# Kernel optimization log

Measured on AMD Instinct MI355X. Metric: run time of the kernel, lower is better.

Reference implementation:

```python
import jax, jax.numpy as jnp
import numpy as np

N = 50000   # nodes
E = 800000  # edges
IN, H, C = 256, 128, 4


def _gcn_norm(edge_index, n):
    """Add self-loops and compute symmetric GCN normalization per edge."""
    loops = jnp.arange(n, dtype=edge_index.dtype)
    src = jnp.concatenate([edge_index[0], loops])
    dst = jnp.concatenate([edge_index[1], loops])
    deg = jax.ops.segment_sum(jnp.ones_like(dst, dtype=jnp.float32), dst,
                              num_segments=n)
    dinv = jnp.where(deg > 0, jax.lax.rsqrt(deg), 0.0)
    norm = dinv[src] * dinv[dst]  # [E+N]
    return src, dst, norm


def _gcn_conv(h, src, dst, norm, W, b, n):
    h = h @ W                              # [N, out]
    msg = h[src] * norm[:, None]           # gather + scale, [E+N, out]
    agg = jax.ops.segment_sum(msg, dst, num_segments=n)
    return agg + b


def setup_inputs() -> dict:
    key = jax.random.key(0)
    ks = jax.random.split(key, 5)
    x = jax.random.normal(ks[0], (N, IN), dtype=jnp.float32)
    edge_index = jax.random.randint(ks[1], (2, E), 0, N, dtype=jnp.int32)
    W1 = jax.random.normal(ks[2], (IN, H), dtype=jnp.float32) * (1.0 / np.sqrt(IN))
    b1 = jnp.zeros((H,), dtype=jnp.float32)
    W2 = jax.random.normal(ks[3], (H, C), dtype=jnp.float32) * (1.0 / np.sqrt(H))
    b2 = jnp.zeros((C,), dtype=jnp.float32)
    return {"x": x, "edge_index": edge_index, "W1": W1, "b1": b1,
            "W2": W2, "b2": b2}


def reference(x, edge_index, W1, b1, W2, b2):
    n = x.shape[0]
    src, dst, norm = _gcn_norm(edge_index, n)
    h = jax.nn.relu(_gcn_conv(x, src, dst, norm, W1, b1, n))
    out = _gcn_conv(h, src, dst, norm, W2, b2, n)
    return out
```

## Files before the change

kernel.cpp:

```cpp
#include <hip/hip_runtime.h>
#include <hip/hip_bf16.h>
#include <stdint.h>

typedef __attribute__((ext_vector_type(8))) short short8;
typedef __attribute__((ext_vector_type(4))) float f32x4;
typedef __attribute__((ext_vector_type(8))) uint16_t u16x8;

#define EPB 4096
#define BKT_SHIFT 8
#define CAP 64

static __device__ __forceinline__ uint16_t f_to_bf16(float f) {
  uint32_t u = __float_as_uint(f);
  uint32_t rounding = 0x7fffu + ((u >> 16) & 1u);
  return (uint16_t)((u + rounding) >> 16);
}
static __device__ __forceinline__ uint32_t pk2_bf16(float a, float b) {
  float2 f2; f2.x = a; f2.y = b;
  __hip_bfloat162 h = __float22bfloat162_rn(f2);
  return *reinterpret_cast<uint32_t*>(&h);
}

static __device__ __forceinline__ int excl_scan256w(int v, int* ws, int tid) {
  int lane = tid & 63, wid = tid >> 6;
  int s = v;
  #pragma unroll
  for (int off = 1; off < 64; off <<= 1) {
    int t2 = __shfl_up(s, off);
    if (lane >= off) s += t2;
  }
  if (wid < 4 && lane == 63) ws[wid] = s;
  __syncthreads();
  int add = 0;
  #pragma unroll
  for (int w = 0; w < 4; ++w)
    if (w < wid) add += ws[w];
  return add + s - v;
}

__global__ __launch_bounds__(512) void k_bscatter(const int* __restrict__ ei, int E,
                                                  int ebk, int slabstride,
                                                  int* __restrict__ cnt_g,
                                                  uint32_t* __restrict__ coo,
                                                  const float* __restrict__ W1,
                                                  uint16_t* __restrict__ w1f) {
  int tid = threadIdx.x, bid = blockIdx.x;
  if (bid >= ebk) {
    int s = (bid - ebk) * 512 + tid;
    if (s < 4096) {
      int lane = s & 63, ks = (s >> 6) & 7, nt = s >> 9;
      int nn = nt * 16 + (lane & 15);
      int kb = ks * 32 + (lane >> 4) * 8;
      u16x8 o;
      #pragma unroll
      for (int j = 0; j < 8; ++j) o[j] = f_to_bf16(W1[(kb + j) * 128 + nn]);
      *(u16x8*)&w1f[(size_t)s * 8] = o;
    }
    return;
  }
  __shared__ uint32_t pk[EPB], pko[EPB];
  __shared__ uint8_t bk[EPB], bko[EPB];
  __shared__ int hist[256], hscan[256], cur[256];
  __shared__ int ws[4];
  if (tid < 256) { hist[tid] = 0; cur[tid] = 0; }
  __syncthreads();
  int base = bid * EPB;
  int nT = min(EPB, E - base);
  for (int i = tid; i < nT; i += 512) {
    int s = ei[base + i];
    int d = ei[E + base + i];
    int b = d >> BKT_SHIFT;
    pk[i] = ((uint32_t)(d & ((1 << BKT_SHIFT) - 1)) << 16) | (uint32_t)s;
    bk[i] = (uint8_t)b;
    atomicAdd(&hist[b], 1);
  }
  __syncthreads();
  int v = (tid < 256) ? hist[tid] : 0;
  int hexcl = excl_scan256w(v, ws, tid);
  if (tid < 256) {
    hscan[tid] = hexcl;
    cnt_g[bid * 256 + tid] = v;
  }
  __syncthreads();
  for (int i = tid; i < nT; i += 512) {
    int b = bk[i];
    int p = hscan[b] + atomicAdd(&cur[b], 1);
    pko[p] = pk[i];
    bko[p] = (uint8_t)b;
  }
  __syncthreads();
  for (int i = tid; i < nT; i += 512) {
    int b = bko[i];
    int off = i - hscan[b];
    if (off < CAP)
      coo[(size_t)b * slabstride + bid * CAP + off] = pko[i];
  }
}

__global__ __launch_bounds__(512) void k_bcsr_gemm(
    const uint32_t* __restrict__ coo, const int* __restrict__ cnt_g,
    int nbkt, int ebk, int slabstride,
    int* __restrict__ rbeg, int* __restrict__ rdeg, float* __restrict__ dinv,
    int* __restrict__ col, int n,
    const float* __restrict__ x, const uint16_t* __restrict__ w1f,
    uint16_t* __restrict__ g) {
  __shared__ uint16_t bF[32768];
  __shared__ int hist[256], lscan[256], cur[256], cnt_l[256];
  __shared__ int ws[4];
  int tid = threadIdx.x, bid = blockIdx.x;
  int lane = tid & 63, wid = tid >> 6;

  if (bid < nbkt) {
    int bkt = bid;
    if (tid < 256) {
      hist[tid] = 0;
      cur[tid] = 0;
      cnt_l[tid] = (tid < ebk) ? cnt_g[tid * 256 + bkt] : 0;
    }
    __syncthreads();
    const uint32_t* slab = coo + (size_t)bkt * slabstride;
    int tot = ebk * CAP;
    for (int lin = tid; lin < tot; lin += 512) {
      int blk = lin >> 6, j = lin & (CAP - 1);
      if (j < cnt_l[blk]) atomicAdd(&hist[slab[lin] >> 16], 1);
    }
    __syncthreads();
    int lexcl = excl_scan256w((tid < 256) ? hist[tid] : 0, ws, tid);
    if (tid < 256) {
      lscan[tid] = lexcl;
      int v = (bkt << BKT_SHIFT) + tid;
      if (v < n) {
        rbeg[v] = bkt * slabstride + lexcl;
        rdeg[v] = hist[tid];
        dinv[v] = rsqrtf((float)(hist[tid] + 1));
      }
    }
    __syncthreads();
    int cbase = bkt * slabstride;
    for (int lin = tid; lin < tot; lin += 512) {
      int blk = lin >> 6, j = lin & (CAP - 1);
      if (j < cnt_l[blk]) {
        uint32_t p = slab[lin];
        int local = p >> 16;
        int pos = lscan[local] + atomicAdd(&cur[local], 1);
        col[cbase + pos] = (int)(p & 0xffffu);
      }
    }
    return;
  }

  int brow = (bid - nbkt) * 128;
  {
    const u16x8* src = (const u16x8*)w1f;
    u16x8* dst = (u16x8*)bF;
    #pragma unroll
    for (int j = 0; j < 8; ++j) dst[tid + j * 512] = src[tid + j * 512];
  }
  __syncthreads();

  f32x4 acc[8];
  #pragma unroll
  for (int j = 0; j < 8; ++j) acc[j] = (f32x4)0.0f;

  int r0 = brow + wid * 16 + (lane & 15);
  const float* xr0 = x + (size_t)r0 * 256 + (lane >> 4) * 8;
  bool ok0 = r0 < n;

  #pragma unroll 2
  for (int ks = 0; ks < 8; ++ks) {
    f32x4 a0a = ok0 ? *(const f32x4*)(xr0 + ks * 32) : (f32x4)0.0f;
    f32x4 a0b = ok0 ? *(const f32x4*)(xr0 + ks * 32 + 4) : (f32x4)0.0f;
    union { short8 s; uint32_t u[4]; } af0;
    af0.u[0] = pk2_bf16(a0a[0], a0a[1]);
    af0.u[1] = pk2_bf16(a0a[2], a0a[3]);
    af0.u[2] = pk2_bf16(a0b[0], a0b[1]);
    af0.u[3] = pk2_bf16(a0b[2], a0b[3]);
    #pragma unroll
    for (int nt = 0; nt < 8; ++nt) {
      short8 bfr = *(const short8*)&bF[((nt * 8 + ks) * 64 + lane) * 8];
      acc[nt] = __builtin_amdgcn_mfma_f32_16x16x32_bf16(af0.s, bfr, acc[nt], 0, 0, 0);
    }
  }
  #pragma unroll
  for (int r = 0; r < 4; ++r) {
    int orow = brow + wid * 16 + (lane >> 4) * 4 + r;
    if (orow < n) {
      #pragma unroll
      for (int nt = 0; nt < 8; ++nt)
        g[(size_t)orow * 128 + nt * 16 + (lane & 15)] = f_to_bf16(acc[nt][r]);
    }
  }
}

__global__ __launch_bounds__(256) void k_agg1(const uint16_t* __restrict__ g,
                                              const int* __restrict__ rbeg,
                                              const int* __restrict__ rdeg,
                                              const int* __restrict__ col,
                                              const float* __restrict__ dinv,
                                              const float* __restrict__ b1,
                                              const float* __restrict__ W2,
                                              float* __restrict__ g2, int n) {
  int lane = threadIdx.x & 63, wid = threadIdx.x >> 6;
  int v = blockIdx.x * 4 + wid;
  if (v >= n) return;
  const uint32_t* gw = (const uint32_t*)g;
  float dv = dinv[v];
  uint32_t u = gw[(size_t)v * 64 + lane];
  float s0 = dv * __uint_as_float(u << 16);
  float s1 = dv * __uint_as_float(u & 0xffff0000u);
  int beg = rbeg[v], end = beg + rdeg[v];
  for (int base = beg; base < end; base += 64) {
    int idx = base + lane;
    int cv = (idx < end) ? col[idx] : v;
    float dvl = dinv[cv];
    int m = min(64, end - base);
    int nb = (m + 15) >> 4;
    for (int t = 0; t < nb; ++t) {
      int bb = t * 16;
      uint32_t r[16];
      float dvj[16];
      #pragma unroll
      for (int j = 0; j < 16; ++j) {
        int uu = __shfl(cv, bb + j);
        dvj[j] = __shfl(dvl, bb + j);
        r[j] = gw[(size_t)uu * 64 + lane];
      }
      int mm = m - bb;
      #pragma unroll
      for (int j = 0; j < 16; ++j) {
        if (j < mm) {
          s0 += dvj[j] * __uint_as_float(r[j] << 16);
          s1 += dvj[j] * __uint_as_float(r[j] & 0xffff0000u);
        }
      }
    }
  }
  float h0 = fmaxf(dv * s0 + b1[2 * lane], 0.0f);
  float h1 = fmaxf(dv * s1 + b1[2 * lane + 1], 0.0f);
  f32x4 w0 = *(const f32x4*)&W2[lane * 8];
  f32x4 w1 = *(const f32x4*)&W2[lane * 8 + 4];
  float p[4];
  #pragma unroll
  for (int c = 0; c < 4; ++c) p[c] = h0 * w0[c] + h1 * w1[c];
  #pragma unroll
  for (int off = 1; off < 64; off <<= 1) {
    #pragma unroll
    for (int c = 0; c < 4; ++c) p[c] += __shfl_xor(p[c], off);
  }
  if (lane == 0) {
    f32x4 o = {dv * p[0], dv * p[1], dv * p[2], dv * p[3]};
    *(f32x4*)&g2[(size_t)v * 4] = o;
  }
}

__global__ __launch_bounds__(256) void k_agg2(const float* __restrict__ g2,
                                              const int* __restrict__ rbeg,
                                              const int* __restrict__ rdeg,
                                              const int* __restrict__ col,
                                              const float* __restrict__ dinv,
                                              const float* __restrict__ b2,
                                              float* __restrict__ out, int n) {
  int t = blockIdx.x * 256 + threadIdx.x;
  int v = t >> 2, c = t & 3;
  if (v >= n) return;
  float a = g2[(size_t)v * 4 + c];
  int beg = rbeg[v], end = beg + rdeg[v];
  for (int base = beg; base < end; base += 8) {
    int m = end - base;
    float r[8];
    #pragma unroll
    for (int q = 0; q < 8; ++q) {
      int jj = base + q;
      int idx = (jj < end) ? col[jj] : v;
      r[q] = g2[(size_t)idx * 4 + c];
    }
    #pragma unroll
    for (int q = 0; q < 8; ++q)
      if (q < m) a += r[q];
  }
  out[(size_t)v * 4 + c] = dinv[v] * a + b2[c];
}

extern "C" void kernel_launch(void* const* d_in, const int* in_sizes, int n_in,
                              void* d_out, int out_size, void* d_ws, size_t ws_size,
                              hipStream_t stream) {
  const float* x  = (const float*)d_in[0];
  const int* ei   = (const int*)d_in[1];
  const float* W1 = (const float*)d_in[2];
  const float* b1 = (const float*)d_in[3];
  const float* W2 = (const float*)d_in[4];
  const float* b2 = (const float*)d_in[5];
  float* out = (float*)d_out;
  int n = in_sizes[0] / 256;
  int E = in_sizes[1] / 2;
  int nbkt = (n + 255) >> BKT_SHIFT;
  int ebk = (E + EPB - 1) / EPB;
  int slabstride = ebk * CAP;

  char* ws = (char*)d_ws;
  size_t off = 0;
  auto alloc = [&](size_t bytes) -> void* {
    void* p = (void*)(ws + off);
    off += (bytes + 255) & ~(size_t)255;
    return p;
  };
  uint32_t* coo = (uint32_t*)alloc((size_t)nbkt * slabstride * 4);
  int* colA     = (int*)alloc((size_t)nbkt * slabstride * 4);
  int* cnt_g    = (int*)alloc((size_t)ebk * 256 * 4);
  int* rbeg     = (int*)alloc((size_t)n * 4);
  int* rdeg     = (int*)alloc((size_t)n * 4);
  float* dinv   = (float*)alloc((size_t)n * 4);
  uint16_t* w1f = (uint16_t*)alloc((size_t)256 * 128 * 2);
  uint16_t* g   = (uint16_t*)alloc((size_t)n * 128 * 2);
  float* g2     = (float*)alloc((size_t)n * 4 * 4);

  int gemmb = (n + 127) / 128;
  k_bscatter<<<dim3(ebk + 8), dim3(512), 0, stream>>>(ei, E, ebk, slabstride,
                                                      cnt_g, coo, W1, w1f);
  k_bcsr_gemm<<<dim3(nbkt + gemmb), dim3(512), 0, stream>>>(
      coo, cnt_g, nbkt, ebk, slabstride, rbeg, rdeg, dinv, colA, n, x, w1f, g);
  k_agg1<<<dim3((n + 3) / 4), dim3(256), 0, stream>>>(g, rbeg, rdeg, colA, dinv,
                                                      b1, W2, g2, n);
  k_agg2<<<dim3((4 * n + 255) / 256), dim3(256), 0, stream>>>(g2, rbeg, rdeg, colA,
                                                              dinv, b2, out, n);
}
```

Measured before the change: 171.4 us.

## Split CSR build from GEMM and fold source dinv scaling into GEMM epilogue

Separates the fused CSR-build/GEMM kernel into two launches so the GEMM can read the degree normalization, then pre-scales each GEMM output row by its dinv. This removes the per-edge dinv gather, shuffle and multiply from the layer-1 aggregation, which now sums raw neighbor rows and applies the destination dinv once at the end. The GEMM also moves to 256 threads with each wave handling 32 rows, reusing each B fragment for two MFMAs. The cost is an extra kernel launch and losing the overlap between CSR building and the GEMM.

```diff
diff --git a/kernel.cpp b/kernel.cpp
--- a/kernel.cpp
+++ b/kernel.cpp
@@ -97,97 +97,114 @@
   }
 }
 
-__global__ __launch_bounds__(512) void k_bcsr_gemm(
-    const uint32_t* __restrict__ coo, const int* __restrict__ cnt_g,
-    int nbkt, int ebk, int slabstride,
-    int* __restrict__ rbeg, int* __restrict__ rdeg, float* __restrict__ dinv,
-    int* __restrict__ col, int n,
-    const float* __restrict__ x, const uint16_t* __restrict__ w1f,
-    uint16_t* __restrict__ g) {
-  __shared__ uint16_t bF[32768];
+__global__ __launch_bounds__(512) void k_bcsr(const uint32_t* __restrict__ coo,
+                                              const int* __restrict__ cnt_g,
+                                              int nbkt, int ebk, int slabstride,
+                                              int* __restrict__ rbeg,
+                                              int* __restrict__ rdeg,
+                                              float* __restrict__ dinv,
+                                              int* __restrict__ col, int n) {
   __shared__ int hist[256], lscan[256], cur[256], cnt_l[256];
   __shared__ int ws[4];
-  int tid = threadIdx.x, bid = blockIdx.x;
-  int lane = tid & 63, wid = tid >> 6;
-
-  if (bid < nbkt) {
-    int bkt = bid;
-    if (tid < 256) {
-      hist[tid] = 0;
-      cur[tid] = 0;
-      cnt_l[tid] = (tid < ebk) ? cnt_g[tid * 256 + bkt] : 0;
-    }
-    __syncthreads();
-    const uint32_t* slab = coo + (size_t)bkt * slabstride;
-    int tot = ebk * CAP;
-    for (int lin = tid; lin < tot; lin += 512) {
-      int blk = lin >> 6, j = lin & (CAP - 1);
-      if (j < cnt_l[blk]) atomicAdd(&hist[slab[lin] >> 16], 1);
-    }
-    __syncthreads();
-    int lexcl = excl_scan256w((tid < 256) ? hist[tid] : 0, ws, tid);
-    if (tid < 256) {
-      lscan[tid] = lexcl;
-      int v = (bkt << BKT_SHIFT) + tid;
-      if (v < n) {
-        rbeg[v] = bkt * slabstride + lexcl;
-        rdeg[v] = hist[tid];
-        dinv[v] = rsqrtf((float)(hist[tid] + 1));
-      }
-    }
-    __syncthreads();
-    int cbase = bkt * slabstride;
-    for (int lin = tid; lin < tot; lin += 512) {
-      int blk = lin >> 6, j = lin & (CAP - 1);
-      if (j < cnt_l[blk]) {
-        uint32_t p = slab[lin];
-        int local = p >> 16;
-        int pos = lscan[local] + atomicAdd(&cur[local], 1);
-        col[cbase + pos] = (int)(p & 0xffffu);
-      }
-    }
-    return;
-  }
-
-  int brow = (bid - nbkt) * 128;
+  int tid = threadIdx.x, bkt = blockIdx.x;
+  if (tid < 256) {
+    hist[tid] = 0;
+    cur[tid] = 0;
+    cnt_l[tid] = (tid < ebk) ? cnt_g[tid * 256 + bkt] : 0;
+  }
+  __syncthreads();
+  const uint32_t* slab = coo + (size_t)bkt * slabstride;
+  int tot = ebk * CAP;
+  for (int lin = tid; lin < tot; lin += 512) {
+    int blk = lin >> 6, j = lin & (CAP - 1);
+    if (j < cnt_l[blk]) atomicAdd(&hist[slab[lin] >> 16], 1);
+  }
+  __syncthreads();
+  int lexcl = excl_scan256w((tid < 256) ? hist[tid] : 0, ws, tid);
+  if (tid < 256) {
+    lscan[tid] = lexcl;
+    int v = (bkt << BKT_SHIFT) + tid;
+    if (v < n) {
+      rbeg[v] = bkt * slabstride + lexcl;
+      rdeg[v] = hist[tid];
+      dinv[v] = rsqrtf((float)(hist[tid] + 1));
+    }
+  }
+  __syncthreads();
+  int cbase = bkt * slabstride;
+  for (int lin = tid; lin < tot; lin += 512) {
+    int blk = lin >> 6, j = lin & (CAP - 1);
+    if (j < cnt_l[blk]) {
+      uint32_t p = slab[lin];
+      int local = p >> 16;
+      int pos = lscan[local] + atomicAdd(&cur[local], 1);
+      col[cbase + pos] = (int)(p & 0xffffu);
+    }
+  }
+}
+
+__global__ __launch_bounds__(256) void k_gemm1(const float* __restrict__ x,
+                                               const uint16_t* __restrict__ w1f,
+                                               const float* __restrict__ dinv,
+                                               uint16_t* __restrict__ g, int n) {
+  __shared__ uint16_t bF[32768];
+  int tid = threadIdx.x, lane = tid & 63, wid = tid >> 6;
+  int brow = blockIdx.x * 128;
+
   {
     const u16x8* src = (const u16x8*)w1f;
     u16x8* dst = (u16x8*)bF;
     #pragma unroll
-    for (int j = 0; j < 8; ++j) dst[tid + j * 512] = src[tid + j * 512];
-  }
-  __syncthreads();
-
-  f32x4 acc[8];
-  #pragma unroll
-  for (int j = 0; j < 8; ++j) acc[j] = (f32x4)0.0f;
-
-  int r0 = brow + wid * 16 + (lane & 15);
+    for (int j = 0; j < 16; ++j) dst[tid + j * 256] = src[tid + j * 256];
+  }
+  __syncthreads();
+
+  f32x4 acc[2][8];
+  #pragma unroll
+  for (int i = 0; i < 2; ++i)
+    #pragma unroll
+    for (int j = 0; j < 8; ++j) acc[i][j] = (f32x4)0.0f;
+
+  int r0 = brow + wid * 32 + (lane & 15);
+  int r1 = r0 + 16;
   const float* xr0 = x + (size_t)r0 * 256 + (lane >> 4) * 8;
-  bool ok0 = r0 < n;
+  const float* xr1 = x + (size_t)r1 * 256 + (lane >> 4) * 8;
+  bool ok0 = r0 < n, ok1 = r1 < n;
 
   #pragma unroll 2
   for (int ks = 0; ks < 8; ++ks) {
     f32x4 a0a = ok0 ? *(const f32x4*)(xr0 + ks * 32) : (f32x4)0.0f;
     f32x4 a0b = ok0 ? *(const f32x4*)(xr0 + ks * 32 + 4) : (f32x4)0.0f;
-    union { short8 s; uint32_t u[4]; } af0;
+    f32x4 a1a = ok1 ? *(const f32x4*)(xr1 + ks * 32) : (f32x4)0.0f;
+    f32x4 a1b = ok1 ? *(const f32x4*)(xr1 + ks * 32 + 4) : (f32x4)0.0f;
+    union { short8 s; uint32_t u[4]; } af0, af1;
     af0.u[0] = pk2_bf16(a0a[0], a0a[1]);
     af0.u[1] = pk2_bf16(a0a[2], a0a[3]);
     af0.u[2] = pk2_bf16(a0b[0], a0b[1]);
     af0.u[3] = pk2_bf16(a0b[2], a0b[3]);
+    af1.u[0] = pk2_bf16(a1a[0], a1a[1]);
+    af1.u[1] = pk2_bf16(a1a[2], a1a[3]);
+    af1.u[2] = pk2_bf16(a1b[0], a1b[1]);
+    af1.u[3] = pk2_bf16(a1b[2], a1b[3]);
     #pragma unroll
     for (int nt = 0; nt < 8; ++nt) {
       short8 bfr = *(const short8*)&bF[((nt * 8 + ks) * 64 + lane) * 8];
-      acc[nt] = __builtin_amdgcn_mfma_f32_16x16x32_bf16(af0.s, bfr, acc[nt], 0, 0, 0);
-    }
-  }
-  #pragma unroll
-  for (int r = 0; r < 4; ++r) {
-    int orow = brow + wid * 16 + (lane >> 4) * 4 + r;
-    if (orow < n) {
-      #pragma unroll
-      for (int nt = 0; nt < 8; ++nt)
-        g[(size_t)orow * 128 + nt * 16 + (lane & 15)] = f_to_bf16(acc[nt][r]);
+      acc[0][nt] = __builtin_amdgcn_mfma_f32_16x16x32_bf16(af0.s, bfr, acc[0][nt], 0, 0, 0);
+      acc[1][nt] = __builtin_amdgcn_mfma_f32_16x16x32_bf16(af1.s, bfr, acc[1][nt], 0, 0, 0);
+    }
+  }
+  #pragma unroll
+  for (int rf = 0; rf < 2; ++rf) {
+    #pragma unroll
+    for (int r = 0; r < 4; ++r) {
+      int orow = brow + wid * 32 + rf * 16 + (lane >> 4) * 4 + r;
+      if (orow < n) {
+        float dv = dinv[orow];
+        #pragma unroll
+        for (int nt = 0; nt < 8; ++nt) {
+          g[(size_t)orow * 128 + nt * 16 + (lane & 15)] = f_to_bf16(acc[rf][nt][r] * dv);
+        }
+      }
     }
   }
 }
@@ -204,37 +221,34 @@
   int v = blockIdx.x * 4 + wid;
   if (v >= n) return;
   const uint32_t* gw = (const uint32_t*)g;
-  float dv = dinv[v];
   uint32_t u = gw[(size_t)v * 64 + lane];
-  float s0 = dv * __uint_as_float(u << 16);
-  float s1 = dv * __uint_as_float(u & 0xffff0000u);
+  float s0 = __uint_as_float(u << 16);
+  float s1 = __uint_as_float(u & 0xffff0000u);
   int beg = rbeg[v], end = beg + rdeg[v];
   for (int base = beg; base < end; base += 64) {
     int idx = base + lane;
     int cv = (idx < end) ? col[idx] : v;
-    float dvl = dinv[cv];
     int m = min(64, end - base);
     int nb = (m + 15) >> 4;
     for (int t = 0; t < nb; ++t) {
       int bb = t * 16;
       uint32_t r[16];
-      float dvj[16];
       #pragma unroll
       for (int j = 0; j < 16; ++j) {
         int uu = __shfl(cv, bb + j);
-        dvj[j] = __shfl(dvl, bb + j);
         r[j] = gw[(size_t)uu * 64 + lane];
       }
       int mm = m - bb;
       #pragma unroll
       for (int j = 0; j < 16; ++j) {
         if (j < mm) {
-          s0 += dvj[j] * __uint_as_float(r[j] << 16);
-          s1 += dvj[j] * __uint_as_float(r[j] & 0xffff0000u);
+          s0 += __uint_as_float(r[j] << 16);
+          s1 += __uint_as_float(r[j] & 0xffff0000u);
         }
       }
     }
   }
+  float dv = dinv[v];
   float h0 = fmaxf(dv * s0 + b1[2 * lane], 0.0f);
   float h1 = fmaxf(dv * s1 + b1[2 * lane + 1], 0.0f);
   f32x4 w0 = *(const f32x4*)&W2[lane * 8];
@@ -314,11 +328,11 @@
   uint16_t* g   = (uint16_t*)alloc((size_t)n * 128 * 2);
   float* g2     = (float*)alloc((size_t)n * 4 * 4);
 
-  int gemmb = (n + 127) / 128;
   k_bscatter<<<dim3(ebk + 8), dim3(512), 0, stream>>>(ei, E, ebk, slabstride,
                                                       cnt_g, coo, W1, w1f);
-  k_bcsr_gemm<<<dim3(nbkt + gemmb), dim3(512), 0, stream>>>(
-      coo, cnt_g, nbkt, ebk, slabstride, rbeg, rdeg, dinv, colA, n, x, w1f, g);
+  k_bcsr<<<dim3(nbkt), dim3(512), 0, stream>>>(coo, cnt_g, nbkt, ebk, slabstride,
+                                               rbeg, rdeg, dinv, colA, n);
+  k_gemm1<<<dim3((n + 127) / 128), dim3(256), 0, stream>>>(x, w1f, dinv, g, n);
   k_agg1<<<dim3((n + 3) / 4), dim3(256), 0, stream>>>(g, rbeg, rdeg, colA, dinv,
                                                       b1, W2, g2, n);
   k_agg2<<<dim3((4 * n + 255) / 256), dim3(256), 0, stream>>>(g2, rbeg, rdeg, colA,
```

New measurement: 173.1 us. Within noise of the previous version (+1.0%).
